# Performance work log

Measured on AMD Instinct MI355X. Metric: run time of the kernel, lower is better.

## Reference

```python
import jax, jax.numpy as jnp
import numpy as np

INF = 1000.0
T = 1.0
NUM_CLASSES = 64


def setup_inputs() -> dict:
    key = jax.random.key(0)
    k1, k2, k3 = jax.random.split(key, 3)
    Nq, Ns, D = 4096, 8192, 256
    xq = jax.random.normal(k1, (Nq, D), dtype=jnp.float32)
    xs = jax.random.normal(k2, (Ns, D), dtype=jnp.float32)
    ys = jax.random.randint(k3, (Ns,), 0, NUM_CLASSES)
    # each query is assumed to be an entry of the support set at position pos[i]
    yq = ys[:Nq]
    pos = jnp.arange(Nq)
    return {"xq": xq, "yq": yq, "xs": xs, "ys": ys, "pos": pos}


def reference(xq, yq, xs, ys, pos):
    Nq = xq.shape[0]
    C = NUM_CLASSES
    # unique(return_counts): classes assumed to be 0..C-1, counts per class
    counts = jax.ops.segment_sum(jnp.ones_like(ys), ys, num_segments=C)  # [C]
    class_mask = yq[:, None] == ys[None, :]                              # [Nq,Ns]
    idx = class_mask.sum(-1) > 1                                         # [Nq]

    # l2_dist: -cdist(xq,xs)^2 / 2, via the |x|^2+|y|^2-2xy expansion (GEMM)
    sq = (jnp.sum(xq * xq, -1, keepdims=True)
          + jnp.sum(xs * xs, -1)[None, :]
          - 2.0 * (xq @ xs.T))
    sq = jnp.maximum(sq, 0.0)
    logit = (-0.5 * sq) / T                                              # [Nq,Ns]

    ind = jnp.arange(Nq)
    # logit[ind,pos] *= 0 ; logit[ind[idx], pos[idx]] -= INF
    logit = logit.at[ind, pos].set(jnp.where(idx, -INF, 0.0))

    # positive logit: masked logsumexp over same-class support columns
    pos_logit = jax.scipy.special.logsumexp(
        logit + jnp.where(class_mask, 0.0, -INF), axis=1, keepdims=True)  # [Nq,1]

    # per-class column segment-sum (the python loop in the original) as one GEMM
    onehot_s = jax.nn.one_hot(ys, C, dtype=logit.dtype)                  # [Ns,C]
    summed = logit @ onehot_s                                            # [Nq,C]

    # adjusted_counts[ind, yq] -= 1
    adj = counts[None, :].astype(logit.dtype) - jax.nn.one_hot(yq, C, dtype=logit.dtype)
    normalized = summed / adj                                            # [Nq,C]
    neg_logit = jax.scipy.special.logsumexp(normalized, axis=1, keepdims=True)

    return jnp.mean(neg_logit - pos_logit)
```

## Files before the change

### kernel.cpp

```cpp
#include <hip/hip_runtime.h>

#define NQ 4096
#define NS 8192
#define DD 256
#define NC 64
#define INFV 1000.0f

typedef __attribute__((ext_vector_type(8))) __bf16 bf16x8;
typedef __attribute__((ext_vector_type(4))) float floatx4;

__device__ inline unsigned short f2bf(float f) {
    unsigned int u = __builtin_bit_cast(unsigned int, f);
    unsigned int r = (u + 0x7FFFu + ((u >> 16) & 1u)) >> 16;
    return (unsigned short)r;
}

__device__ inline bf16x8 cvt8(const float* p) {
    unsigned short tmp[8];
#pragma unroll
    for (int i = 0; i < 8; ++i) tmp[i] = f2bf(p[i]);
    return *(bf16x8*)tmp;
}

__global__ __launch_bounds__(256) void k_prep_hist(const float* __restrict__ xq,
                                                   const float* __restrict__ xs,
                                                   const int* __restrict__ ys,
                                                   unsigned short* __restrict__ xqh,
                                                   unsigned short* __restrict__ xsh,
                                                   float* __restrict__ nq2,
                                                   float* __restrict__ ns2,
                                                   float* __restrict__ ldot,
                                                   int* __restrict__ counts,
                                                   int* __restrict__ qcounts,
                                                   int* __restrict__ soff,
                                                   int* __restrict__ qoff,
                                                   int* __restrict__ sperm,
                                                   int* __restrict__ qperm) {
    __shared__ int h4[4][NC], hq4[4][NC], wb4[4][NC], wbq4[4][NC];

    if (blockIdx.x == 0) {
        const int tid = threadIdx.x;
        const int wave = tid >> 6;
        ((int*)h4)[tid] = 0;
        ((int*)hq4)[tid] = 0;
        __syncthreads();
        int v[32];
#pragma unroll
        for (int i = 0; i < 16; ++i) {
            int j = tid + i * 256;
            v[i] = ys[j];
            atomicAdd(&h4[wave][v[i]], 1);
            atomicAdd(&hq4[wave][v[i]], 1);
        }
#pragma unroll
        for (int i = 16; i < 32; ++i) {
            int j = tid + i * 256;
            v[i] = ys[j];
            atomicAdd(&h4[wave][v[i]], 1);
        }
        __syncthreads();
        if (tid < NC) {
            const int c = tid;
            int tot = 0, totq = 0;
            int pre[4], preq[4];
#pragma unroll
            for (int w = 0; w < 4; ++w) {
                pre[w] = tot; preq[w] = totq;
                tot += h4[w][c]; totq += hq4[w][c];
            }
            counts[c] = tot; qcounts[c] = totq;
            int x = tot, xb = totq;
#pragma unroll
            for (int off = 1; off < 64; off <<= 1) {
                int y0 = __shfl_up(x, off, 64);
                int y1 = __shfl_up(xb, off, 64);
                if (c >= off) { x += y0; xb += y1; }
            }
            int base = x - tot, baseq = xb - totq;
            soff[c] = base; qoff[c] = baseq;
#pragma unroll
            for (int w = 0; w < 4; ++w) {
                wb4[w][c] = base + pre[w];
                wbq4[w][c] = baseq + preq[w];
            }
        }
        __syncthreads();
#pragma unroll
        for (int i = 0; i < 16; ++i) {
            int j = tid + i * 256;
            int c = v[i];
            sperm[atomicAdd(&wb4[wave][c], 1)] = j;
            qperm[atomicAdd(&wbq4[wave][c], 1)] = j;
        }
#pragma unroll
        for (int i = 16; i < 32; ++i) {
            int j = tid + i * 256;
            int c = v[i];
            sperm[atomicAdd(&wb4[wave][c], 1)] = j;
        }
        return;
    }

    int row = (blockIdx.x - 1) * 4 + (threadIdx.x >> 6);
    int lane = threadIdx.x & 63;
    if (row < NQ) {
        float4 v = ((const float4*)(xq + (size_t)row * DD))[lane];
        float4 b = ((const float4*)(xs + (size_t)row * DD))[lane];
        float s = v.x * v.x + v.y * v.y + v.z * v.z + v.w * v.w;
        float d = v.x * b.x + v.y * b.y + v.z * b.z + v.w * b.w;
        ((ushort4*)(xqh + (size_t)row * DD))[lane] =
            make_ushort4(f2bf(v.x), f2bf(v.y), f2bf(v.z), f2bf(v.w));
#pragma unroll
        for (int off = 32; off; off >>= 1) {
            s += __shfl_xor(s, off, 64);
            d += __shfl_xor(d, off, 64);
        }
        if (lane == 0) { nq2[row] = s; ldot[row] = d; }
    } else {
        int r = row - NQ;
        float4 v = ((const float4*)(xs + (size_t)r * DD))[lane];
        float s = v.x * v.x + v.y * v.y + v.z * v.z + v.w * v.w;
        ((ushort4*)(xsh + (size_t)r * DD))[lane] =
            make_ushort4(f2bf(v.x), f2bf(v.y), f2bf(v.z), f2bf(v.w));
#pragma unroll
        for (int off = 32; off; off >>= 1) s += __shfl_xor(s, off, 64);
        if (lane == 0) ns2[r] = s;
    }
}

__global__ __launch_bounds__(256) void k_cent_pos(const float* __restrict__ xs,
                                                  const unsigned short* __restrict__ xqh,
                                                  const unsigned short* __restrict__ xsh,
                                                  const float* __restrict__ nq2,
                                                  const float* __restrict__ ns2,
                                                  const int* __restrict__ counts,
                                                  const int* __restrict__ qcounts,
                                                  const int* __restrict__ soff,
                                                  const int* __restrict__ qoff,
                                                  const int* __restrict__ sperm,
                                                  const int* __restrict__ qperm,
                                                  float* __restrict__ mcent,
                                                  float* __restrict__ Sc,
                                                  float* __restrict__ poslog) {
    __shared__ float redc[4][256];
    __shared__ float sredc[4];
    __shared__ int qish[16];
    __shared__ float nqsh[16];
    __shared__ float msh[4][16], ssh[4][16];

    const int c = blockIdx.x;
    const int qc = qcounts[c];
    const int mc = counts[c];
    const int sbase = soff[c];
    const int qbase = qoff[c];
    const float ov = (mc > 1) ? -INFV : 0.0f;

    const int tid = threadIdx.x;
    const int lane = tid & 63;
    const int wave = tid >> 6;
    const int quad = lane >> 4;
    const int l15 = lane & 15;

    if (blockIdx.y == 0) {
        float4 acc = make_float4(0.f, 0.f, 0.f, 0.f);
        float sacc = 0.0f;
        for (int idx = wave; idx < mc; idx += 4) {
            int row = sperm[sbase + idx];
            float4 v = ((const float4*)(xs + (size_t)row * DD))[lane];
            acc.x += v.x; acc.y += v.y; acc.z += v.z; acc.w += v.w;
            if (lane == 0) sacc += ns2[row];
        }
        ((float4*)redc[wave])[lane] = acc;
        if (lane == 0) sredc[wave] = sacc;
        __syncthreads();
        if (wave == 0) {
            int k0 = lane * 4;
#pragma unroll
            for (int j = 0; j < 4; ++j) {
                mcent[(size_t)c * DD + k0 + j] =
                    redc[0][k0 + j] + redc[1][k0 + j] + redc[2][k0 + j] + redc[3][k0 + j];
            }
            if (lane == 0) Sc[c] = sredc[0] + sredc[1] + sredc[2] + sredc[3];
        }
    }

    for (int q0 = blockIdx.y * 16; q0 < qc; q0 += gridDim.y * 16) {
        __syncthreads();
        if (tid < 16) {
            int idx = q0 + tid;
            int qi = (idx < qc) ? qperm[qbase + idx] : -1;
            qish[tid] = qi;
            nqsh[tid] = (qi >= 0) ? nq2[qi] : 0.0f;
        }
        __syncthreads();

        int qrow = qish[l15];
        int qrowL = qrow < 0 ? 0 : qrow;
        const unsigned short* ap = xqh + (size_t)qrowL * DD + quad * 8;
        bf16x8 afr[8];
#pragma unroll
        for (int ks = 0; ks < 8; ++ks) afr[ks] = *(const bf16x8*)(ap + ks * 32);

        int qid[4];
        float nqr[4];
#pragma unroll
        for (int r = 0; r < 4; ++r) {
            qid[r] = qish[quad * 4 + r];
            nqr[r] = nqsh[quad * 4 + r];
        }

        float mrun[4], srun[4];
#pragma unroll
        for (int r = 0; r < 4; ++r) { mrun[r] = -1e30f; srun[r] = 0.0f; }

        for (int jt = wave * 16; jt < mc; jt += 64) {
            int jcol = jt + l15;
            bool valid = jcol < mc;
            int sj = valid ? sperm[sbase + jcol] : -1;
            int sjL = sj < 0 ? 0 : sj;
            float nsv = valid ? ns2[sjL] : 0.0f;
            const unsigned short* bp = xsh + (size_t)sjL * DD + quad * 8;
            floatx4 acc = (floatx4)0.0f;
#pragma unroll
            for (int ks = 0; ks < 8; ++ks) {
                bf16x8 bfr = *(const bf16x8*)(bp + ks * 32);
                acc = __builtin_amdgcn_mfma_f32_16x16x32_bf16(afr[ks], bfr, acc, 0, 0, 0);
            }
            if (valid) {
#pragma unroll
                for (int r = 0; r < 4; ++r) {
                    float v = fminf(acc[r] - 0.5f * (nqr[r] + nsv), 0.0f);
                    if (sj == qid[r]) v = ov;
                    float mn = fmaxf(mrun[r], v);
                    srun[r] = srun[r] * __expf(mrun[r] - mn) + __expf(v - mn);
                    mrun[r] = mn;
                }
            }
        }
#pragma unroll
        for (int r = 0; r < 4; ++r) {
#pragma unroll
            for (int off = 1; off < 16; off <<= 1) {
                float m2 = __shfl_xor(mrun[r], off, 64);
                float s2 = __shfl_xor(srun[r], off, 64);
                float mn = fmaxf(mrun[r], m2);
                srun[r] = srun[r] * __expf(mrun[r] - mn) + s2 * __expf(m2 - mn);
                mrun[r] = mn;
            }
            if (l15 == 0) {
                msh[wave][quad * 4 + r] = mrun[r];
                ssh[wave][quad * 4 + r] = srun[r];
            }
        }
        __syncthreads();
        if (tid < 16) {
            int qi = qish[tid];
            if (qi >= 0) {
                float m = -1e30f, s = 0.0f;
#pragma unroll
                for (int w = 0; w < 4; ++w) {
                    float mw = msh[w][tid], sw = ssh[w][tid];
                    float mn = fmaxf(m, mw);
                    s = s * __expf(m - mn) + sw * __expf(mw - mn);
                    m = mn;
                }
                poslog[qi] = m + __logf(s);
            }
        }
    }
}

__global__ __launch_bounds__(256) void k_final(const unsigned short* __restrict__ xqh,
                                               const float* __restrict__ mcent,
                                               const float* __restrict__ Sc,
                                               const int* __restrict__ counts,
                                               const int* __restrict__ yq,
                                               const float* __restrict__ nq2,
                                               const float* __restrict__ ns2,
                                               const float* __restrict__ ldot,
                                               const float* __restrict__ poslog,
                                               float* __restrict__ out) {
    __shared__ float cntf[64], scs[64], nqs[64], ldts[64], ns2s[64], pls[64], red[64];
    __shared__ int ysh[64];

    const int b = blockIdx.x;
    const int tid = threadIdx.x;
    const int lane = tid & 63;
    const int wave = tid >> 6;
    const int quad = lane >> 4;
    const int l15 = lane & 15;

    if (tid < 64) {
        cntf[tid] = (float)counts[tid];
        scs[tid] = Sc[tid];
        int row = b * 64 + tid;
        nqs[tid] = nq2[row];
        ysh[tid] = yq[row];
        ldts[tid] = ldot[row];
        ns2s[tid] = ns2[row];
        pls[tid] = poslog[row];
    }
    __syncthreads();

    const unsigned short* ap = xqh + (size_t)(b * 64 + wave * 16 + l15) * DD + quad * 8;
    bf16x8 afr[8];
#pragma unroll
    for (int ks = 0; ks < 8; ++ks) afr[ks] = *(const bf16x8*)(ap + ks * 32);

    floatx4 acc[4];
#pragma unroll
    for (int n = 0; n < 4; ++n) acc[n] = (floatx4)0.0f;

#pragma unroll
    for (int n = 0; n < 4; ++n) {
        const float* bp = mcent + (size_t)(n * 16 + l15) * DD + quad * 8;
#pragma unroll
        for (int ks = 0; ks < 8; ++ks) {
            bf16x8 bfr = cvt8(bp + ks * 32);
            acc[n] = __builtin_amdgcn_mfma_f32_16x16x32_bf16(afr[ks], bfr, acc[n], 0, 0, 0);
        }
    }

#pragma unroll
    for (int r = 0; r < 4; ++r) {
        int rl = wave * 16 + quad * 4 + r;
        float nqv = nqs[rl];
        int y = ysh[rl];
        float vv[4];
#pragma unroll
        for (int n = 0; n < 4; ++n) {
            int col = n * 16 + l15;
            float cnt = cntf[col];
            float val = acc[n][r] - 0.5f * cnt * nqv - 0.5f * scs[col];
            float sub = (col == y) ? 1.0f : 0.0f;
            if (col == y) {
                float lii = ldts[rl] - 0.5f * (nqv + ns2s[rl]);
                val += ((cnt > 1.5f) ? -INFV : 0.0f) - lii;
            }
            vv[n] = val / (cnt - sub);
        }
        float m = fmaxf(fmaxf(vv[0], vv[1]), fmaxf(vv[2], vv[3]));
#pragma unroll
        for (int off = 1; off < 16; off <<= 1) m = fmaxf(m, __shfl_xor(m, off, 64));
        float e = __expf(vv[0] - m) + __expf(vv[1] - m) + __expf(vv[2] - m) +
                  __expf(vv[3] - m);
#pragma unroll
        for (int off = 1; off < 16; off <<= 1) e += __shfl_xor(e, off, 64);
        if (l15 == 0) red[rl] = (m + __logf(e) - pls[rl]) * (1.0f / (float)NQ);
    }
    __syncthreads();
    if (tid < 64) {
        float s = red[tid];
#pragma unroll
        for (int off = 32; off; off >>= 1) s += __shfl_xor(s, off, 64);
        if (tid == 0) atomicAdd(out, s);
    }
}

extern "C" void kernel_launch(void* const* d_in, const int* in_sizes, int n_in,
                              void* d_out, int out_size, void* d_ws, size_t ws_size,
                              hipStream_t stream) {
    const float* xq = (const float*)d_in[0];
    const int* yq = (const int*)d_in[1];
    const float* xs = (const float*)d_in[2];
    const int* ys = (const int*)d_in[3];
    float* out = (float*)d_out;
    char* ws = (char*)d_ws;

    unsigned short* xqh = (unsigned short*)(ws + 0);
    unsigned short* xsh = (unsigned short*)(ws + 2097152);
    float* nq2 = (float*)(ws + 6291456);
    float* ns2 = (float*)(ws + 6307840);
    int* counts = (int*)(ws + 6340608);
    int* qcounts = (int*)(ws + 6340864);
    int* soff = (int*)(ws + 6341120);
    int* qoff = (int*)(ws + 6341376);
    int* sperm = (int*)(ws + 6341632);
    int* qperm = (int*)(ws + 6374400);
    float* poslog = (float*)(ws + 6390784);
    float* ldot = (float*)(ws + 6407168);
    float* mcent = (float*)(ws + 6423552);
    float* Sc = (float*)(ws + 6489088);

    hipMemsetAsync(d_out, 0, (size_t)out_size * 4, stream);

    k_prep_hist<<<dim3((NQ + NS) / 4 + 1), dim3(256), 0, stream>>>(
        xq, xs, ys, xqh, xsh, nq2, ns2, ldot, counts, qcounts, soff, qoff, sperm, qperm);
    k_cent_pos<<<dim3(NC, 8), dim3(256), 0, stream>>>(xs, xqh, xsh, nq2, ns2, counts,
                                                      qcounts, soff, qoff, sperm, qperm,
                                                      mcent, Sc, poslog);
    k_final<<<dim3(64), dim3(256), 0, stream>>>(xqh, mcent, Sc, counts, yq, nq2, ns2,
                                                ldot, poslog, out);
}
```

Baseline: 127.9 us.

## Fuse three kernels into one cooperative kernel with grid syncs and dynamic work queue

Merges the prep/histogram, centroid/positive-logit and final kernels into a single cooperative launch of 512 blocks separated by grid.sync, removing two kernel launch boundaries. Centroid accumulation is split across four blocks per class with atomic adds, and positive-logit query tiles are handed out through an atomic work queue built during the histogram phase to balance uneven class sizes. The cost is grid-wide barriers, float atomics (order nondeterminism), and fewer blocks active in later phases.

```diff
diff --git a/kernel.cpp b/kernel.cpp
--- a/kernel.cpp
+++ b/kernel.cpp
@@ -1,10 +1,15 @@
 #include <hip/hip_runtime.h>
+#include <hip/hip_cooperative_groups.h>
+
+namespace cg = cooperative_groups;
 
 #define NQ 4096
 #define NS 8192
 #define DD 256
 #define NC 64
 #define INFV 1000.0f
+#define NBLK 512
+#define CONVBLK (NBLK - 1)
 
 typedef __attribute__((ext_vector_type(8))) __bf16 bf16x8;
 typedef __attribute__((ext_vector_type(4))) float floatx4;
@@ -22,25 +27,36 @@
     return *(bf16x8*)tmp;
 }
 
-__global__ __launch_bounds__(256) void k_prep_hist(const float* __restrict__ xq,
-                                                   const float* __restrict__ xs,
-                                                   const int* __restrict__ ys,
-                                                   unsigned short* __restrict__ xqh,
-                                                   unsigned short* __restrict__ xsh,
-                                                   float* __restrict__ nq2,
-                                                   float* __restrict__ ns2,
-                                                   float* __restrict__ ldot,
-                                                   int* __restrict__ counts,
-                                                   int* __restrict__ qcounts,
-                                                   int* __restrict__ soff,
-                                                   int* __restrict__ qoff,
-                                                   int* __restrict__ sperm,
-                                                   int* __restrict__ qperm) {
+__global__ __launch_bounds__(256, 2) void k_fused(
+    const float* __restrict__ xq, const int* __restrict__ yq,
+    const float* __restrict__ xs, const int* __restrict__ ys,
+    unsigned short* __restrict__ xqh, unsigned short* __restrict__ xsh,
+    float* __restrict__ nq2, float* __restrict__ ns2, float* __restrict__ ldot,
+    int* __restrict__ counts, int* __restrict__ qcounts, int* __restrict__ soff,
+    int* __restrict__ qoff, int* __restrict__ sperm, int* __restrict__ qperm,
+    float* __restrict__ mcent, float* __restrict__ Sc, float* __restrict__ poslog,
+    int* __restrict__ qcur, int* __restrict__ nunits, int* __restrict__ workq,
+    float* __restrict__ out) {
+    cg::grid_group grid = cg::this_grid();
+
     __shared__ int h4[4][NC], hq4[4][NC], wb4[4][NC], wbq4[4][NC];
-
-    if (blockIdx.x == 0) {
-        const int tid = threadIdx.x;
-        const int wave = tid >> 6;
+    __shared__ float redc[4][256];
+    __shared__ float sredc[4];
+    __shared__ int qish[16];
+    __shared__ float nqsh[16];
+    __shared__ float msh[4][16], ssh[4][16];
+    __shared__ int ush;
+    __shared__ float cntf[64], scs[64], nqs[64], ldts[64], ns2s[64], pls[64], red[64];
+    __shared__ int ysh[64];
+
+    const int b = blockIdx.x;
+    const int tid = threadIdx.x;
+    const int lane = tid & 63;
+    const int wave = tid >> 6;
+    const int quad = lane >> 4;
+    const int l15 = lane & 15;
+
+    if (b == 0) {
         ((int*)h4)[tid] = 0;
         ((int*)hq4)[tid] = 0;
         __syncthreads();
@@ -69,20 +85,25 @@
                 tot += h4[w][c]; totq += hq4[w][c];
             }
             counts[c] = tot; qcounts[c] = totq;
-            int x = tot, xb = totq;
+            int ntile = (totq + 15) >> 4;
+            int x = tot, xb = totq, tb = ntile;
 #pragma unroll
             for (int off = 1; off < 64; off <<= 1) {
                 int y0 = __shfl_up(x, off, 64);
                 int y1 = __shfl_up(xb, off, 64);
-                if (c >= off) { x += y0; xb += y1; }
-            }
-            int base = x - tot, baseq = xb - totq;
+                int y2 = __shfl_up(tb, off, 64);
+                if (c >= off) { x += y0; xb += y1; tb += y2; }
+            }
+            int base = x - tot, baseq = xb - totq, tbase = tb - ntile;
             soff[c] = base; qoff[c] = baseq;
 #pragma unroll
             for (int w = 0; w < 4; ++w) {
                 wb4[w][c] = base + pre[w];
                 wbq4[w][c] = baseq + preq[w];
             }
+            for (int t = 0; t < ntile; ++t) workq[tbase + t] = (c << 16) | t;
+            if (c == NC - 1) *nunits = tbase + ntile;
+            if (c == 0) *qcur = 0;
         }
         __syncthreads();
 #pragma unroll
@@ -98,73 +119,49 @@
             int c = v[i];
             sperm[atomicAdd(&wb4[wave][c], 1)] = j;
         }
-        return;
+    } else {
+        if (b <= NC) {
+            if (tid < 64)
+                ((float4*)(mcent + (size_t)(b - 1) * DD))[tid] =
+                    make_float4(0.f, 0.f, 0.f, 0.f);
+            if (tid == 64) Sc[b - 1] = 0.0f;
+        }
+        for (int row = (b - 1) * 4 + wave; row < NQ + NS; row += CONVBLK * 4) {
+            if (row < NQ) {
+                float4 v = ((const float4*)(xq + (size_t)row * DD))[lane];
+                float4 bb = ((const float4*)(xs + (size_t)row * DD))[lane];
+                float s = v.x * v.x + v.y * v.y + v.z * v.z + v.w * v.w;
+                float d = v.x * bb.x + v.y * bb.y + v.z * bb.z + v.w * bb.w;
+                ((ushort4*)(xqh + (size_t)row * DD))[lane] =
+                    make_ushort4(f2bf(v.x), f2bf(v.y), f2bf(v.z), f2bf(v.w));
+#pragma unroll
+                for (int off = 32; off; off >>= 1) {
+                    s += __shfl_xor(s, off, 64);
+                    d += __shfl_xor(d, off, 64);
+                }
+                if (lane == 0) { nq2[row] = s; ldot[row] = d; }
+            } else {
+                int r = row - NQ;
+                float4 v = ((const float4*)(xs + (size_t)r * DD))[lane];
+                float s = v.x * v.x + v.y * v.y + v.z * v.z + v.w * v.w;
+                ((ushort4*)(xsh + (size_t)r * DD))[lane] =
+                    make_ushort4(f2bf(v.x), f2bf(v.y), f2bf(v.z), f2bf(v.w));
+#pragma unroll
+                for (int off = 32; off; off >>= 1) s += __shfl_xor(s, off, 64);
+                if (lane == 0) ns2[r] = s;
+            }
+        }
     }
-
-    int row = (blockIdx.x - 1) * 4 + (threadIdx.x >> 6);
-    int lane = threadIdx.x & 63;
-    if (row < NQ) {
-        float4 v = ((const float4*)(xq + (size_t)row * DD))[lane];
-        float4 b = ((const float4*)(xs + (size_t)row * DD))[lane];
-        float s = v.x * v.x + v.y * v.y + v.z * v.z + v.w * v.w;
-        float d = v.x * b.x + v.y * b.y + v.z * b.z + v.w * b.w;
-        ((ushort4*)(xqh + (size_t)row * DD))[lane] =
-            make_ushort4(f2bf(v.x), f2bf(v.y), f2bf(v.z), f2bf(v.w));
-#pragma unroll
-        for (int off = 32; off; off >>= 1) {
-            s += __shfl_xor(s, off, 64);
-            d += __shfl_xor(d, off, 64);
-        }
-        if (lane == 0) { nq2[row] = s; ldot[row] = d; }
-    } else {
-        int r = row - NQ;
-        float4 v = ((const float4*)(xs + (size_t)r * DD))[lane];
-        float s = v.x * v.x + v.y * v.y + v.z * v.z + v.w * v.w;
-        ((ushort4*)(xsh + (size_t)r * DD))[lane] =
-            make_ushort4(f2bf(v.x), f2bf(v.y), f2bf(v.z), f2bf(v.w));
-#pragma unroll
-        for (int off = 32; off; off >>= 1) s += __shfl_xor(s, off, 64);
-        if (lane == 0) ns2[r] = s;
-    }
-}
-
-__global__ __launch_bounds__(256) void k_cent_pos(const float* __restrict__ xs,
-                                                  const unsigned short* __restrict__ xqh,
-                                                  const unsigned short* __restrict__ xsh,
-                                                  const float* __restrict__ nq2,
-                                                  const float* __restrict__ ns2,
-                                                  const int* __restrict__ counts,
-                                                  const int* __restrict__ qcounts,
-                                                  const int* __restrict__ soff,
-                                                  const int* __restrict__ qoff,
-                                                  const int* __restrict__ sperm,
-                                                  const int* __restrict__ qperm,
-                                                  float* __restrict__ mcent,
-                                                  float* __restrict__ Sc,
-                                                  float* __restrict__ poslog) {
-    __shared__ float redc[4][256];
-    __shared__ float sredc[4];
-    __shared__ int qish[16];
-    __shared__ float nqsh[16];
-    __shared__ float msh[4][16], ssh[4][16];
-
-    const int c = blockIdx.x;
-    const int qc = qcounts[c];
-    const int mc = counts[c];
-    const int sbase = soff[c];
-    const int qbase = qoff[c];
-    const float ov = (mc > 1) ? -INFV : 0.0f;
-
-    const int tid = threadIdx.x;
-    const int lane = tid & 63;
-    const int wave = tid >> 6;
-    const int quad = lane >> 4;
-    const int l15 = lane & 15;
-
-    if (blockIdx.y == 0) {
+    grid.sync();
+
+    if (b < 256) {
+        const int c = b >> 2;
+        const int yb = b & 3;
+        const int mc = counts[c];
+        const int sbase = soff[c];
         float4 acc = make_float4(0.f, 0.f, 0.f, 0.f);
         float sacc = 0.0f;
-        for (int idx = wave; idx < mc; idx += 4) {
+        for (int idx = yb * 4 + wave; idx < mc; idx += 16) {
             int row = sperm[sbase + idx];
             float4 v = ((const float4*)(xs + (size_t)row * DD))[lane];
             acc.x += v.x; acc.y += v.y; acc.z += v.z; acc.w += v.w;
@@ -177,15 +174,30 @@
             int k0 = lane * 4;
 #pragma unroll
             for (int j = 0; j < 4; ++j) {
-                mcent[(size_t)c * DD + k0 + j] =
-                    redc[0][k0 + j] + redc[1][k0 + j] + redc[2][k0 + j] + redc[3][k0 + j];
-            }
-            if (lane == 0) Sc[c] = sredc[0] + sredc[1] + sredc[2] + sredc[3];
+                float v = redc[0][k0 + j] + redc[1][k0 + j] + redc[2][k0 + j] +
+                          redc[3][k0 + j];
+                atomicAdd(&mcent[(size_t)c * DD + k0 + j], v);
+            }
+            if (lane == 0) atomicAdd(&Sc[c], sredc[0] + sredc[1] + sredc[2] + sredc[3]);
         }
     }
 
-    for (int q0 = blockIdx.y * 16; q0 < qc; q0 += gridDim.y * 16) {
-        __syncthreads();
+    const int NU = *nunits;
+    while (true) {
+        __syncthreads();
+        if (tid == 0) ush = atomicAdd(qcur, 1);
+        __syncthreads();
+        int u = ush;
+        if (u >= NU) break;
+        const int c = workq[u] >> 16;
+        const int t = workq[u] & 0xffff;
+        const int qc = qcounts[c];
+        const int mc = counts[c];
+        const int sbase = soff[c];
+        const int qbase = qoff[c];
+        const float ov = (mc > 1) ? -INFV : 0.0f;
+        const int q0 = t * 16;
+
         if (tid < 16) {
             int idx = q0 + tid;
             int qi = (idx < qc) ? qperm[qbase + idx] : -1;
@@ -268,92 +280,76 @@
             }
         }
     }
-}
-
-__global__ __launch_bounds__(256) void k_final(const unsigned short* __restrict__ xqh,
-                                               const float* __restrict__ mcent,
-                                               const float* __restrict__ Sc,
-                                               const int* __restrict__ counts,
-                                               const int* __restrict__ yq,
-                                               const float* __restrict__ nq2,
-                                               const float* __restrict__ ns2,
-                                               const float* __restrict__ ldot,
-                                               const float* __restrict__ poslog,
-                                               float* __restrict__ out) {
-    __shared__ float cntf[64], scs[64], nqs[64], ldts[64], ns2s[64], pls[64], red[64];
-    __shared__ int ysh[64];
-
-    const int b = blockIdx.x;
-    const int tid = threadIdx.x;
-    const int lane = tid & 63;
-    const int wave = tid >> 6;
-    const int quad = lane >> 4;
-    const int l15 = lane & 15;
-
-    if (tid < 64) {
-        cntf[tid] = (float)counts[tid];
-        scs[tid] = Sc[tid];
-        int row = b * 64 + tid;
-        nqs[tid] = nq2[row];
-        ysh[tid] = yq[row];
-        ldts[tid] = ldot[row];
-        ns2s[tid] = ns2[row];
-        pls[tid] = poslog[row];
-    }
-    __syncthreads();
-
-    const unsigned short* ap = xqh + (size_t)(b * 64 + wave * 16 + l15) * DD + quad * 8;
-    bf16x8 afr[8];
-#pragma unroll
-    for (int ks = 0; ks < 8; ++ks) afr[ks] = *(const bf16x8*)(ap + ks * 32);
-
-    floatx4 acc[4];
-#pragma unroll
-    for (int n = 0; n < 4; ++n) acc[n] = (floatx4)0.0f;
-
-#pragma unroll
-    for (int n = 0; n < 4; ++n) {
-        const float* bp = mcent + (size_t)(n * 16 + l15) * DD + quad * 8;
-#pragma unroll
-        for (int ks = 0; ks < 8; ++ks) {
-            bf16x8 bfr = cvt8(bp + ks * 32);
-            acc[n] = __builtin_amdgcn_mfma_f32_16x16x32_bf16(afr[ks], bfr, acc[n], 0, 0, 0);
-        }
-    }
-
-#pragma unroll
-    for (int r = 0; r < 4; ++r) {
-        int rl = wave * 16 + quad * 4 + r;
-        float nqv = nqs[rl];
-        int y = ysh[rl];
-        float vv[4];
+    grid.sync();
+
+    if (b < 64) {
+        if (tid < 64) {
+            cntf[tid] = (float)counts[tid];
+            scs[tid] = Sc[tid];
+            int row = b * 64 + tid;
+            nqs[tid] = nq2[row];
+            ysh[tid] = yq[row];
+            ldts[tid] = ldot[row];
+            ns2s[tid] = ns2[row];
+            pls[tid] = poslog[row];
+        }
+        __syncthreads();
+
+        const unsigned short* ap =
+            xqh + (size_t)(b * 64 + wave * 16 + l15) * DD + quad * 8;
+        bf16x8 afr[8];
+#pragma unroll
+        for (int ks = 0; ks < 8; ++ks) afr[ks] = *(const bf16x8*)(ap + ks * 32);
+
+        floatx4 acc[4];
+#pragma unroll
+        for (int n = 0; n < 4; ++n) acc[n] = (floatx4)0.0f;
+
 #pragma unroll
         for (int n = 0; n < 4; ++n) {
-            int col = n * 16 + l15;
-            float cnt = cntf[col];
-            float val = acc[n][r] - 0.5f * cnt * nqv - 0.5f * scs[col];
-            float sub = (col == y) ? 1.0f : 0.0f;
-            if (col == y) {
-                float lii = ldts[rl] - 0.5f * (nqv + ns2s[rl]);
-                val += ((cnt > 1.5f) ? -INFV : 0.0f) - lii;
-            }
-            vv[n] = val / (cnt - sub);
-        }
-        float m = fmaxf(fmaxf(vv[0], vv[1]), fmaxf(vv[2], vv[3]));
-#pragma unroll
-        for (int off = 1; off < 16; off <<= 1) m = fmaxf(m, __shfl_xor(m, off, 64));
-        float e = __expf(vv[0] - m) + __expf(vv[1] - m) + __expf(vv[2] - m) +
-                  __expf(vv[3] - m);
-#pragma unroll
-        for (int off = 1; off < 16; off <<= 1) e += __shfl_xor(e, off, 64);
-        if (l15 == 0) red[rl] = (m + __logf(e) - pls[rl]) * (1.0f / (float)NQ);
-    }
-    __syncthreads();
-    if (tid < 64) {
-        float s = red[tid];
-#pragma unroll
-        for (int off = 32; off; off >>= 1) s += __shfl_xor(s, off, 64);
-        if (tid == 0) atomicAdd(out, s);
+            const float* bp = mcent + (size_t)(n * 16 + l15) * DD + quad * 8;
+#pragma unroll
+            for (int ks = 0; ks < 8; ++ks) {
+                bf16x8 bfr = cvt8(bp + ks * 32);
+                acc[n] =
+                    __builtin_amdgcn_mfma_f32_16x16x32_bf16(afr[ks], bfr, acc[n], 0, 0, 0);
+            }
+        }
+
+#pragma unroll
+        for (int r = 0; r < 4; ++r) {
+            int rl = wave * 16 + quad * 4 + r;
+            float nqv = nqs[rl];
+            int y = ysh[rl];
+            float vv[4];
+#pragma unroll
+            for (int n = 0; n < 4; ++n) {
+                int col = n * 16 + l15;
+                float cnt = cntf[col];
+                float val = acc[n][r] - 0.5f * cnt * nqv - 0.5f * scs[col];
+                float sub = (col == y) ? 1.0f : 0.0f;
+                if (col == y) {
+                    float lii = ldts[rl] - 0.5f * (nqv + ns2s[rl]);
+                    val += ((cnt > 1.5f) ? -INFV : 0.0f) - lii;
+                }
+                vv[n] = val / (cnt - sub);
+            }
+            float m = fmaxf(fmaxf(vv[0], vv[1]), fmaxf(vv[2], vv[3]));
+#pragma unroll
+            for (int off = 1; off < 16; off <<= 1) m = fmaxf(m, __shfl_xor(m, off, 64));
+            float e = __expf(vv[0] - m) + __expf(vv[1] - m) + __expf(vv[2] - m) +
+                      __expf(vv[3] - m);
+#pragma unroll
+            for (int off = 1; off < 16; off <<= 1) e += __shfl_xor(e, off, 64);
+            if (l15 == 0) red[rl] = (m + __logf(e) - pls[rl]) * (1.0f / (float)NQ);
+        }
+        __syncthreads();
+        if (tid < 64) {
+            float s = red[tid];
+#pragma unroll
+            for (int off = 32; off; off >>= 1) s += __shfl_xor(s, off, 64);
+            if (tid == 0) atomicAdd(out, s);
+        }
     }
 }
 
@@ -381,14 +377,16 @@
     float* ldot = (float*)(ws + 6407168);
     float* mcent = (float*)(ws + 6423552);
     float* Sc = (float*)(ws + 6489088);
+    int* qcur = (int*)(ws + 6489344);
+    int* nunits = (int*)(ws + 6489348);
+    int* workq = (int*)(ws + 6489600);
 
     hipMemsetAsync(d_out, 0, (size_t)out_size * 4, stream);
 
-    k_prep_hist<<<dim3((NQ + NS) / 4 + 1), dim3(256), 0, stream>>>(
-        xq, xs, ys, xqh, xsh, nq2, ns2, ldot, counts, qcounts, soff, qoff, sperm, qperm);
-    k_cent_pos<<<dim3(NC, 8), dim3(256), 0, stream>>>(xs, xqh, xsh, nq2, ns2, counts,
-                                                      qcounts, soff, qoff, sperm, qperm,
-                                                      mcent, Sc, poslog);
-    k_final<<<dim3(64), dim3(256), 0, stream>>>(xqh, mcent, Sc, counts, yq, nq2, ns2,
-                                                ldot, poslog, out);
+    void* kargs[] = {&xq,     &yq,   &xs,     &ys,   &xqh,    &xsh,  &nq2,
+                     &ns2,    &ldot, &counts, &qcounts, &soff, &qoff, &sperm,
+                     &qperm,  &mcent, &Sc,    &poslog, &qcur, &nunits, &workq,
+                     &out};
+    hipLaunchCooperativeKernel((const void*)k_fused, dim3(NBLK), dim3(256), kargs, 0,
+                               stream);
 }
```

Measured after the change: 256.4 us. 100% more time.

## Flatten positive-logit work into a per-tile queue and split centroid sums across blocks

Applied to the files above, without the earlier changes.

The histogram block now builds a work queue of 16-query tiles per class, and k_cent_pos launches a flat grid. There, 256 blocks compute class centroid partial sums with atomic adds and the remaining blocks each process one queue tile. This replaces the fixed 64x8 grid, where per-class loops and the centroid work sat on the y=0 blocks and caused load imbalance. The output and centroid zeroing moves into the prep kernel, removing the separate memset. Atomic float adds make the centroid sums order-nondeterministic, and the queue bound of 576 blocks assumes at most 320 tiles.

```diff
diff --git a/kernel.cpp b/kernel.cpp
--- a/kernel.cpp
+++ b/kernel.cpp
@@ -35,11 +35,17 @@
                                                    int* __restrict__ soff,
                                                    int* __restrict__ qoff,
                                                    int* __restrict__ sperm,
-                                                   int* __restrict__ qperm) {
+                                                   int* __restrict__ qperm,
+                                                   int* __restrict__ nunits,
+                                                   int* __restrict__ workq,
+                                                   float* __restrict__ mcent,
+                                                   float* __restrict__ Sc,
+                                                   float* __restrict__ out, int osz) {
     __shared__ int h4[4][NC], hq4[4][NC], wb4[4][NC], wbq4[4][NC];
-
-    if (blockIdx.x == 0) {
-        const int tid = threadIdx.x;
+    const int tid = threadIdx.x;
+    const int b = blockIdx.x;
+
+    if (b == 0) {
         const int wave = tid >> 6;
         ((int*)h4)[tid] = 0;
         ((int*)hq4)[tid] = 0;
@@ -69,20 +75,24 @@
                 tot += h4[w][c]; totq += hq4[w][c];
             }
             counts[c] = tot; qcounts[c] = totq;
-            int x = tot, xb = totq;
+            int ntile = (totq + 15) >> 4;
+            int x = tot, xb = totq, tb = ntile;
 #pragma unroll
             for (int off = 1; off < 64; off <<= 1) {
                 int y0 = __shfl_up(x, off, 64);
                 int y1 = __shfl_up(xb, off, 64);
-                if (c >= off) { x += y0; xb += y1; }
-            }
-            int base = x - tot, baseq = xb - totq;
+                int y2 = __shfl_up(tb, off, 64);
+                if (c >= off) { x += y0; xb += y1; tb += y2; }
+            }
+            int base = x - tot, baseq = xb - totq, tbase = tb - ntile;
             soff[c] = base; qoff[c] = baseq;
 #pragma unroll
             for (int w = 0; w < 4; ++w) {
                 wb4[w][c] = base + pre[w];
                 wbq4[w][c] = baseq + preq[w];
             }
+            for (int t = 0; t < ntile; ++t) workq[tbase + t] = (c << 16) | t;
+            if (c == NC - 1) *nunits = tbase + ntile;
         }
         __syncthreads();
 #pragma unroll
@@ -101,13 +111,22 @@
         return;
     }
 
-    int row = (blockIdx.x - 1) * 4 + (threadIdx.x >> 6);
-    int lane = threadIdx.x & 63;
+    if (b <= NC) {
+        if (tid < 64)
+            ((float4*)(mcent + (size_t)(b - 1) * DD))[tid] = make_float4(0.f, 0.f, 0.f, 0.f);
+        if (tid == 64) Sc[b - 1] = 0.0f;
+    }
+    if (b == 65) {
+        for (int i = tid; i < osz; i += 256) out[i] = 0.0f;
+    }
+
+    int row = (b - 1) * 4 + (tid >> 6);
+    int lane = tid & 63;
     if (row < NQ) {
         float4 v = ((const float4*)(xq + (size_t)row * DD))[lane];
-        float4 b = ((const float4*)(xs + (size_t)row * DD))[lane];
+        float4 bb = ((const float4*)(xs + (size_t)row * DD))[lane];
         float s = v.x * v.x + v.y * v.y + v.z * v.z + v.w * v.w;
-        float d = v.x * b.x + v.y * b.y + v.z * b.z + v.w * b.w;
+        float d = v.x * bb.x + v.y * bb.y + v.z * bb.z + v.w * bb.w;
         ((ushort4*)(xqh + (size_t)row * DD))[lane] =
             make_ushort4(f2bf(v.x), f2bf(v.y), f2bf(v.z), f2bf(v.w));
 #pragma unroll
@@ -139,6 +158,8 @@
                                                   const int* __restrict__ qoff,
                                                   const int* __restrict__ sperm,
                                                   const int* __restrict__ qperm,
+                                                  const int* __restrict__ nunits,
+                                                  const int* __restrict__ workq,
                                                   float* __restrict__ mcent,
                                                   float* __restrict__ Sc,
                                                   float* __restrict__ poslog) {
@@ -148,124 +169,133 @@
     __shared__ float nqsh[16];
     __shared__ float msh[4][16], ssh[4][16];
 
-    const int c = blockIdx.x;
+    const int b = blockIdx.x;
+    const int tid = threadIdx.x;
+    const int lane = tid & 63;
+    const int wave = tid >> 6;
+    const int quad = lane >> 4;
+    const int l15 = lane & 15;
+
+    if (b < 256) {
+        const int c = b >> 2;
+        const int yb = b & 3;
+        const int mc = counts[c];
+        const int sbase = soff[c];
+        float4 acc = make_float4(0.f, 0.f, 0.f, 0.f);
+        float sacc = 0.0f;
+        for (int idx = yb * 4 + wave; idx < mc; idx += 16) {
+            int row = sperm[sbase + idx];
+            float4 v = ((const float4*)(xs + (size_t)row * DD))[lane];
+            acc.x += v.x; acc.y += v.y; acc.z += v.z; acc.w += v.w;
+            if (lane == 0) sacc += ns2[row];
+        }
+        ((float4*)redc[wave])[lane] = acc;
+        if (lane == 0) sredc[wave] = sacc;
+        __syncthreads();
+        if (wave == 0) {
+            int k0 = lane * 4;
+#pragma unroll
+            for (int j = 0; j < 4; ++j) {
+                float v = redc[0][k0 + j] + redc[1][k0 + j] + redc[2][k0 + j] +
+                          redc[3][k0 + j];
+                atomicAdd(&mcent[(size_t)c * DD + k0 + j], v);
+            }
+            if (lane == 0) atomicAdd(&Sc[c], sredc[0] + sredc[1] + sredc[2] + sredc[3]);
+        }
+        return;
+    }
+
+    const int NU = *nunits;
+    const int u = b - 256;
+    if (u >= NU) return;
+    const int c = workq[u] >> 16;
+    const int t = workq[u] & 0xffff;
     const int qc = qcounts[c];
     const int mc = counts[c];
     const int sbase = soff[c];
     const int qbase = qoff[c];
     const float ov = (mc > 1) ? -INFV : 0.0f;
-
-    const int tid = threadIdx.x;
-    const int lane = tid & 63;
-    const int wave = tid >> 6;
-    const int quad = lane >> 4;
-    const int l15 = lane & 15;
-
-    if (blockIdx.y == 0) {
-        float4 acc = make_float4(0.f, 0.f, 0.f, 0.f);
-        float sacc = 0.0f;
-        for (int idx = wave; idx < mc; idx += 4) {
-            int row = sperm[sbase + idx];
-            float4 v = ((const float4*)(xs + (size_t)row * DD))[lane];
-            acc.x += v.x; acc.y += v.y; acc.z += v.z; acc.w += v.w;
-            if (lane == 0) sacc += ns2[row];
-        }
-        ((float4*)redc[wave])[lane] = acc;
-        if (lane == 0) sredc[wave] = sacc;
-        __syncthreads();
-        if (wave == 0) {
-            int k0 = lane * 4;
-#pragma unroll
-            for (int j = 0; j < 4; ++j) {
-                mcent[(size_t)c * DD + k0 + j] =
-                    redc[0][k0 + j] + redc[1][k0 + j] + redc[2][k0 + j] + redc[3][k0 + j];
-            }
-            if (lane == 0) Sc[c] = sredc[0] + sredc[1] + sredc[2] + sredc[3];
-        }
-    }
-
-    for (int q0 = blockIdx.y * 16; q0 < qc; q0 += gridDim.y * 16) {
-        __syncthreads();
-        if (tid < 16) {
-            int idx = q0 + tid;
-            int qi = (idx < qc) ? qperm[qbase + idx] : -1;
-            qish[tid] = qi;
-            nqsh[tid] = (qi >= 0) ? nq2[qi] : 0.0f;
-        }
-        __syncthreads();
-
-        int qrow = qish[l15];
-        int qrowL = qrow < 0 ? 0 : qrow;
-        const unsigned short* ap = xqh + (size_t)qrowL * DD + quad * 8;
-        bf16x8 afr[8];
-#pragma unroll
-        for (int ks = 0; ks < 8; ++ks) afr[ks] = *(const bf16x8*)(ap + ks * 32);
-
-        int qid[4];
-        float nqr[4];
-#pragma unroll
-        for (int r = 0; r < 4; ++r) {
-            qid[r] = qish[quad * 4 + r];
-            nqr[r] = nqsh[quad * 4 + r];
-        }
-
-        float mrun[4], srun[4];
-#pragma unroll
-        for (int r = 0; r < 4; ++r) { mrun[r] = -1e30f; srun[r] = 0.0f; }
-
-        for (int jt = wave * 16; jt < mc; jt += 64) {
-            int jcol = jt + l15;
-            bool valid = jcol < mc;
-            int sj = valid ? sperm[sbase + jcol] : -1;
-            int sjL = sj < 0 ? 0 : sj;
-            float nsv = valid ? ns2[sjL] : 0.0f;
-            const unsigned short* bp = xsh + (size_t)sjL * DD + quad * 8;
-            floatx4 acc = (floatx4)0.0f;
-#pragma unroll
-            for (int ks = 0; ks < 8; ++ks) {
-                bf16x8 bfr = *(const bf16x8*)(bp + ks * 32);
-                acc = __builtin_amdgcn_mfma_f32_16x16x32_bf16(afr[ks], bfr, acc, 0, 0, 0);
-            }
-            if (valid) {
-#pragma unroll
-                for (int r = 0; r < 4; ++r) {
-                    float v = fminf(acc[r] - 0.5f * (nqr[r] + nsv), 0.0f);
-                    if (sj == qid[r]) v = ov;
-                    float mn = fmaxf(mrun[r], v);
-                    srun[r] = srun[r] * __expf(mrun[r] - mn) + __expf(v - mn);
-                    mrun[r] = mn;
-                }
-            }
-        }
-#pragma unroll
-        for (int r = 0; r < 4; ++r) {
-#pragma unroll
-            for (int off = 1; off < 16; off <<= 1) {
-                float m2 = __shfl_xor(mrun[r], off, 64);
-                float s2 = __shfl_xor(srun[r], off, 64);
-                float mn = fmaxf(mrun[r], m2);
-                srun[r] = srun[r] * __expf(mrun[r] - mn) + s2 * __expf(m2 - mn);
+    const int q0 = t * 16;
+
+    if (tid < 16) {
+        int idx = q0 + tid;
+        int qi = (idx < qc) ? qperm[qbase + idx] : -1;
+        qish[tid] = qi;
+        nqsh[tid] = (qi >= 0) ? nq2[qi] : 0.0f;
+    }
+    __syncthreads();
+
+    int qrow = qish[l15];
+    int qrowL = qrow < 0 ? 0 : qrow;
+    const unsigned short* ap = xqh + (size_t)qrowL * DD + quad * 8;
+    bf16x8 afr[8];
+#pragma unroll
+    for (int ks = 0; ks < 8; ++ks) afr[ks] = *(const bf16x8*)(ap + ks * 32);
+
+    int qid[4];
+    float nqr[4];
+#pragma unroll
+    for (int r = 0; r < 4; ++r) {
+        qid[r] = qish[quad * 4 + r];
+        nqr[r] = nqsh[quad * 4 + r];
+    }
+
+    float mrun[4], srun[4];
+#pragma unroll
+    for (int r = 0; r < 4; ++r) { mrun[r] = -1e30f; srun[r] = 0.0f; }
+
+    for (int jt = wave * 16; jt < mc; jt += 64) {
+        int jcol = jt + l15;
+        bool valid = jcol < mc;
+        int sj = valid ? sperm[sbase + jcol] : -1;
+        int sjL = sj < 0 ? 0 : sj;
+        float nsv = valid ? ns2[sjL] : 0.0f;
+        const unsigned short* bp = xsh + (size_t)sjL * DD + quad * 8;
+        floatx4 acc = (floatx4)0.0f;
+#pragma unroll
+        for (int ks = 0; ks < 8; ++ks) {
+            bf16x8 bfr = *(const bf16x8*)(bp + ks * 32);
+            acc = __builtin_amdgcn_mfma_f32_16x16x32_bf16(afr[ks], bfr, acc, 0, 0, 0);
+        }
+        if (valid) {
+#pragma unroll
+            for (int r = 0; r < 4; ++r) {
+                float v = fminf(acc[r] - 0.5f * (nqr[r] + nsv), 0.0f);
+                if (sj == qid[r]) v = ov;
+                float mn = fmaxf(mrun[r], v);
+                srun[r] = srun[r] * __expf(mrun[r] - mn) + __expf(v - mn);
                 mrun[r] = mn;
             }
-            if (l15 == 0) {
-                msh[wave][quad * 4 + r] = mrun[r];
-                ssh[wave][quad * 4 + r] = srun[r];
-            }
-        }
-        __syncthreads();
-        if (tid < 16) {
-            int qi = qish[tid];
-            if (qi >= 0) {
-                float m = -1e30f, s = 0.0f;
-#pragma unroll
-                for (int w = 0; w < 4; ++w) {
-                    float mw = msh[w][tid], sw = ssh[w][tid];
-                    float mn = fmaxf(m, mw);
-                    s = s * __expf(m - mn) + sw * __expf(mw - mn);
-                    m = mn;
-                }
-                poslog[qi] = m + __logf(s);
-            }
+        }
+    }
+#pragma unroll
+    for (int r = 0; r < 4; ++r) {
+#pragma unroll
+        for (int off = 1; off < 16; off <<= 1) {
+            float m2 = __shfl_xor(mrun[r], off, 64);
+            float s2 = __shfl_xor(srun[r], off, 64);
+            float mn = fmaxf(mrun[r], m2);
+            srun[r] = srun[r] * __expf(mrun[r] - mn) + s2 * __expf(m2 - mn);
+            mrun[r] = mn;
+        }
+        if (l15 == 0) {
+            msh[wave][quad * 4 + r] = mrun[r];
+            ssh[wave][quad * 4 + r] = srun[r];
+        }
+    }
+    __syncthreads();
+    if (tid < 16) {
+        int qi = qish[tid];
+        if (qi >= 0) {
+            float m = -1e30f, s = 0.0f;
+#pragma unroll
+            for (int w = 0; w < 4; ++w) {
+                float mw = msh[w][tid], sw = ssh[w][tid];
+                float mn = fmaxf(m, mw);
+                s = s * __expf(m - mn) + sw * __expf(mw - mn);
+                m = mn;
+            }
+            poslog[qi] = m + __logf(s);
         }
     }
 }
@@ -381,14 +411,15 @@
     float* ldot = (float*)(ws + 6407168);
     float* mcent = (float*)(ws + 6423552);
     float* Sc = (float*)(ws + 6489088);
-
-    hipMemsetAsync(d_out, 0, (size_t)out_size * 4, stream);
+    int* nunits = (int*)(ws + 6489348);
+    int* workq = (int*)(ws + 6489600);
 
     k_prep_hist<<<dim3((NQ + NS) / 4 + 1), dim3(256), 0, stream>>>(
-        xq, xs, ys, xqh, xsh, nq2, ns2, ldot, counts, qcounts, soff, qoff, sperm, qperm);
-    k_cent_pos<<<dim3(NC, 8), dim3(256), 0, stream>>>(xs, xqh, xsh, nq2, ns2, counts,
-                                                      qcounts, soff, qoff, sperm, qperm,
-                                                      mcent, Sc, poslog);
+        xq, xs, ys, xqh, xsh, nq2, ns2, ldot, counts, qcounts, soff, qoff, sperm,
+        qperm, nunits, workq, mcent, Sc, out, out_size);
+    k_cent_pos<<<dim3(576), dim3(256), 0, stream>>>(xs, xqh, xsh, nq2, ns2, counts,
+                                                    qcounts, soff, qoff, sperm, qperm,
+                                                    nunits, workq, mcent, Sc, poslog);
     k_final<<<dim3(64), dim3(256), 0, stream>>>(xqh, mcent, Sc, counts, yq, nq2, ns2,
                                                 ldot, poslog, out);
 }
```

After: 107.2 us. 16.3% less time.
